# Optimization experiments

Measured on AMD Instinct MI355X. Metric: run time of the kernel, lower is better.

The kernel has to match this reference:

```python
import jax, jax.numpy as jnp
import numpy as np
from jax import lax

PRE_NMS = 2000
POST_NMS = 300
NMS_THRESH = 0.7
MIN_SIZE = 16.0
SCALE = 1.0
RATIOS = (0.5, 1.0, 2.0)
SCALES = (8, 16, 32)
STRIDES = (8, 16, 32)
FEAT_HW = ((100, 100), (50, 50), (25, 25))
BASE_SIZE = 16.0


def _anchor_base(scale):
    py = px = BASE_SIZE / 2.0
    ab = np.zeros((len(RATIOS), 4), dtype=np.float32)
    for i, r in enumerate(RATIOS):
        h = BASE_SIZE * scale * np.sqrt(r)
        w = BASE_SIZE * scale * np.sqrt(1.0 / r)
        ab[i] = [py - h / 2.0, px - w / 2.0, py + h / 2.0, px + w / 2.0]
    return ab


def _enum_anchors():
    out = []
    for lvl in range(3):
        ab = _anchor_base(SCALES[lvl])
        hh, ww = FEAT_HW[lvl]
        fs = STRIDES[lvl]
        sy = np.arange(0, hh * fs, fs)
        sx = np.arange(0, ww * fs, fs)
        sx, sy = np.meshgrid(sx, sy)
        shift = np.stack((sy.ravel(), sx.ravel(), sy.ravel(), sx.ravel()), axis=1)
        a = ab[None, :, :] + shift[:, None, :]  # [K, A, 4]
        out.append(a.reshape(-1, 4).astype(np.float32))
    return np.concatenate(out, axis=0)  # [39375, 4]


def setup_inputs() -> dict:
    key = jax.random.key(0)
    ks = jax.random.split(key, 8)
    inp = {
        "feat0": jax.random.normal(ks[0], (2, 256, 100, 100), jnp.float32),
        "feat1": jax.random.normal(ks[1], (2, 256, 50, 50), jnp.float32),
        "feat2": jax.random.normal(ks[2], (2, 256, 25, 25), jnp.float32),
        "conv_w": 0.01 * jax.random.normal(ks[3], (256, 256, 3, 3), jnp.float32),
        "conv_b": jnp.zeros((256,), jnp.float32),
        "score_w": 0.01 * jax.random.normal(ks[4], (6, 256), jnp.float32),
        "score_b": jnp.zeros((6,), jnp.float32),
        "loc_w": 0.01 * jax.random.normal(ks[5], (12, 256), jnp.float32),
        "loc_b": jnp.zeros((12,), jnp.float32),
        "anchors": jnp.asarray(_enum_anchors()),
        "img_h": 800,
        "img_w": 800,
    }
    return inp


def loc2bbox(anchors, loc):
    src_h = anchors[:, 2] - anchors[:, 0]
    src_w = anchors[:, 3] - anchors[:, 1]
    ctr_y = anchors[:, 0] + 0.5 * src_h
    ctr_x = anchors[:, 1] + 0.5 * src_w
    dy, dx, dh, dw = loc[:, 0], loc[:, 1], loc[:, 2], loc[:, 3]
    cy = dy * src_h + ctr_y
    cx = dx * src_w + ctr_x
    h = jnp.exp(dh) * src_h
    w = jnp.exp(dw) * src_w
    return jnp.stack([cy - 0.5 * h, cx - 0.5 * w, cy + 0.5 * h, cx + 0.5 * w], axis=1)


def _iou_matrix(boxes):
    area = (boxes[:, 2] - boxes[:, 0]) * (boxes[:, 3] - boxes[:, 1])
    tl = jnp.maximum(boxes[:, None, :2], boxes[None, :, :2])
    br = jnp.minimum(boxes[:, None, 2:], boxes[None, :, 2:])
    wh = jnp.clip(br - tl, 0.0)
    inter = wh[..., 0] * wh[..., 1]
    return inter / (area[:, None] + area[None, :] - inter + 1e-12)


def _nms_keep(boxes, valid):
    # greedy NMS over score-sorted boxes; returns boolean keep mask
    M = _iou_matrix(boxes)  # [PRE_NMS, PRE_NMS]
    idx = jnp.arange(PRE_NMS)

    def body(i, suppressed):
        sup_later = (~suppressed[i]) & (M[i] > NMS_THRESH) & (idx > i)
        return suppressed | sup_later

    suppressed = lax.fori_loop(0, PRE_NMS, body, ~valid)
    return ~suppressed


def _propose(loc, fg, anchors, img_h, img_w):
    roi = loc2bbox(anchors, loc)  # [S, 4]
    roi = jnp.stack([
        jnp.clip(roi[:, 0], 0.0, float(img_h)),
        jnp.clip(roi[:, 1], 0.0, float(img_w)),
        jnp.clip(roi[:, 2], 0.0, float(img_h)),
        jnp.clip(roi[:, 3], 0.0, float(img_w)),
    ], axis=1)
    hs = roi[:, 2] - roi[:, 0]
    ws = roi[:, 3] - roi[:, 1]
    valid = (hs >= MIN_SIZE * SCALE) & (ws >= MIN_SIZE * SCALE)
    sc = jnp.where(valid, fg, -jnp.inf)
    top_sc, top_idx = lax.top_k(sc, PRE_NMS)
    boxes = roi[top_idx]
    keep = _nms_keep(boxes, jnp.isfinite(top_sc))
    # stable move of kept boxes to the front (indices are unique)
    order = jnp.argsort(jnp.where(keep, jnp.arange(PRE_NMS), PRE_NMS))[:POST_NMS]
    rois = boxes[order] * keep[order][:, None].astype(boxes.dtype)  # zero-pad invalid
    return rois  # [POST_NMS, 4]


def reference(feat0, feat1, feat2, conv_w, conv_b, score_w, score_b, loc_w, loc_b, anchors, img_h, img_w):
    feats = [feat0, feat1, feat2]
    n = feat0.shape[0]
    locs, scores, fgs = [], [], []
    dn = ("NCHW", "OIHW", "NCHW")
    for x in feats:
        h = jax.nn.relu(
            lax.conv_general_dilated(x, conv_w, (1, 1), "SAME", dimension_numbers=dn)
            + conv_b[None, :, None, None]
        )
        hh, ww = h.shape[2], h.shape[3]
        loc = jnp.einsum("nchw,oc->nhwo", h, loc_w) + loc_b  # [n,h,w,12]
        sc = jnp.einsum("nchw,oc->nhwo", h, score_w) + score_b  # [n,h,w,6]
        fg = jax.nn.softmax(sc.reshape(n, hh, ww, 3, 2), axis=-1)[..., 1]
        locs.append(loc.reshape(n, -1, 4))
        scores.append(sc.reshape(n, -1, 2))
        fgs.append(fg.reshape(n, -1))
    rpn_locs = jnp.concatenate(locs, axis=1)      # [n, S, 4]
    rpn_scores = jnp.concatenate(scores, axis=1)  # [n, S, 2]
    rpn_fg = jnp.concatenate(fgs, axis=1)         # [n, S]
    rois = jax.vmap(lambda l, f: _propose(l, f, anchors, img_h, img_w))(rpn_locs, rpn_fg)
    rois = rois.reshape(-1, 4)  # [n*POST_NMS, 4]
    roi_indices = jnp.repeat(jnp.arange(n, dtype=jnp.int32), POST_NMS)
    return rpn_locs, rpn_scores, rois, roi_indices, anchors
```

## Files before the change

### kernel.cpp

```cpp
#include <hip/hip_runtime.h>
#include <hip/hip_fp16.h>
#include <cstdint>
#include <cstddef>

typedef unsigned long long u64;
typedef unsigned int u32;
typedef __attribute__((ext_vector_type(8))) _Float16 f16x8;
typedef __attribute__((ext_vector_type(4))) float f32x4;

#define NANCHORS 39375
#define PRE_NMS  2000
#define POST_NMS 300
#define CAND_CAP 4096
#define MPAD 2048
#define UNEG 0x007FFFFFu
#define NPIX 26250

__device__ __forceinline__ u32 f2u(float f) {
  u32 u = __float_as_uint(f);
  return (u & 0x80000000u) ? ~u : (u | 0x80000000u);
}

#define GLOAD16(gp, lp) __builtin_amdgcn_global_load_lds( \
    (const __attribute__((address_space(1))) u32*)(const void*)(gp), \
    (__attribute__((address_space(3))) u32*)(void*)(lp), 16, 0, 0)

#define DPP_SUM16(v) do { \
  v += __int_as_float(__builtin_amdgcn_update_dpp(0, __float_as_int(v), 0x128, 0xf, 0xf, true)); \
  v += __int_as_float(__builtin_amdgcn_update_dpp(0, __float_as_int(v), 0x124, 0xf, 0xf, true)); \
  v += __int_as_float(__builtin_amdgcn_update_dpp(0, __float_as_int(v), 0x122, 0xf, 0xf, true)); \
  v += __int_as_float(__builtin_amdgcn_update_dpp(0, __float_as_int(v), 0x121, 0xf, 0xf, true)); \
} while (0)

__global__ __launch_bounds__(256) void prep_kernel(
    const float* __restrict__ f0, const float* __restrict__ f1, const float* __restrict__ f2,
    const float* __restrict__ w, const float* __restrict__ anchors,
    short* __restrict__ xh, short* __restrict__ xl,
    short* __restrict__ wh, short* __restrict__ wl,
    float* __restrict__ out_anchors)
{
  int blk = blockIdx.x;
  int tid = threadIdx.x;
  if (blk < 1656) {
    __shared__ float tile[64][65];
    int t = blk;
    int HW, W, W2, np; const float* fp; int AB, ABS;
    if (t < 1256)      { HW = 10000; W = 100; W2 = 102; np = 157; fp = f0; AB = 0;       ABS = 2663424; }
    else if (t < 1576) { t -= 1256; HW = 2500; W = 50; W2 = 52; np = 40; fp = f1; AB = 5326848; ABS = 692224; }
    else               { t -= 1576; HW = 625;  W = 25; W2 = 27; np = 10; fp = f2; AB = 6711296; ABS = 186624; }
    int posb = t % np, r = t / np;
    int ci0 = (r & 3) * 64, b = r >> 2;
    int pos0 = posb * 64;
    int lane = tid & 63, wv = tid >> 6;
    int rp = pos0 + lane; if (rp >= HW) rp = HW - 1;
    const float* src = fp + (size_t)(b * 256 + ci0) * HW;
#pragma unroll
    for (int p = 0; p < 16; ++p) {
      int cl = wv * 16 + p;
      tile[cl][lane] = src[(size_t)cl * HW + rp];
    }
    __syncthreads();
    int pix = tid >> 2, cq = tid & 3;
    int pos = pos0 + pix;
    if (pos < HW) {
      int y = pos / W, x = pos - y * W;
      size_t ob = (size_t)AB + (size_t)b * ABS + ((size_t)((y + 1) * W2 + (x + 1))) * 256 + ci0 + cq * 16;
      __align__(16) short hs[16], ls[16];
#pragma unroll
      for (int j = 0; j < 16; ++j) {
        float v = tile[cq * 16 + j][pix];
        __half h = __float2half(v);
        __half l = __float2half((v - __half2float(h)) * 2048.0f);
        hs[j] = __half_as_short(h);
        ls[j] = __half_as_short(l);
      }
      *(int4*)(xh + ob) = ((int4*)hs)[0];
      *(int4*)(xh + ob + 8) = ((int4*)hs)[1];
      *(int4*)(xl + ob) = ((int4*)ls)[0];
      *(int4*)(xl + ob + 8) = ((int4*)ls)[1];
    }
  } else if (blk < 3960) {
    int idx = (blk - 1656) * 256 + tid;
    int tap = idx >> 16, co = (idx >> 8) & 255, ci = idx & 255;
    float v = w[(size_t)co * 2304 + ci * 9 + tap];
    __half h = __float2half(v);
    __half l = __float2half((v - __half2float(h)) * 2048.0f);
    wh[idx] = __half_as_short(h);
    wl[idx] = __half_as_short(l);
  } else if (blk < 4316) {
    int g = (blk - 3960) * 256 + tid;
    int t = g >> 6, ln = g & 63;
    int b = t / 712, i = t % 712;
    int W2, AB, ABS;
    if (i < 404)      { W2 = 102; AB = 0;       ABS = 2663424; }
    else if (i < 608) { i -= 404; W2 = 52; AB = 5326848; ABS = 692224; }
    else              { i -= 608; W2 = 27; AB = 6711296; ABS = 186624; }
    int y, x;
    if (i < W2)          { y = 0;      x = i; }
    else if (i < 2 * W2) { y = W2 - 1; x = i - W2; }
    else { int j = i - 2 * W2; y = 1 + (j >> 1); x = (j & 1) ? (W2 - 1) : 0; }
    size_t base = (size_t)AB + (size_t)b * ABS + ((size_t)(y * W2 + x)) * 256 + ln * 4;
    int2 z = {0, 0};
    *(int2*)(xh + base) = z;
    *(int2*)(xl + base) = z;
  } else {
    int t = (blk - 4316) * 256 + tid;
    if (t < 157500) out_anchors[t] = anchors[t];
  }
}

__global__ __launch_bounds__(256, 2) void gemmconv_kernel(
    const short* __restrict__ xh, const short* __restrict__ xl,
    const short* __restrict__ wh, const short* __restrict__ wl,
    const float* __restrict__ bias,
    const float* __restrict__ loc_w, const float* __restrict__ score_w,
    float* __restrict__ proj2)
{
  __shared__ __align__(16) short smem[32768];

  int lb = (blockIdx.x & 7) * 52 + (blockIdx.x >> 3);
  int HW, W, W2, AB, ABS, lvlbase;
  if (lb < 316)      { HW = 10000; W = 100; W2 = 102; AB = 0;       ABS = 2663424; lvlbase = 0; }
  else if (lb < 396) { lb -= 316; HW = 2500; W = 50; W2 = 52; AB = 5326848; ABS = 692224; lvlbase = 10000; }
  else               { lb -= 396; HW = 625;  W = 25; W2 = 27; AB = 6711296; ABS = 186624; lvlbase = 12500; }
  int mb = lb >> 2, b = (lb >> 1) & 1, nb = lb & 1;
  int pos0 = mb * 128, co0 = nb * 128;

  int tid = threadIdx.x;
  int s = tid & 7, mrow = tid >> 3;
  int aoff[4], boff[4];
#pragma unroll
  for (int i = 0; i < 4; ++i) {
    int m = i * 32 + mrow;
    int pos = pos0 + m; if (pos >= HW) pos = HW - 1;
    int y = pos / W, x = pos - y * W;
    aoff[i] = AB + b * ABS + (y * W2 + x) * 256 + ((s ^ (m & 7)) << 3);
    boff[i] = ((co0 + m) << 8) + ((s ^ (m & 7)) << 3);
  }
  int wv = tid >> 6, lane = tid & 63;
  int lr = lane & 15, lk = lane >> 4;
  int wr = wv >> 1, wc = wv & 1;
  int rA0 = wr * 64 + lr, rB0 = wc * 64 + lr;
  int cs = (lr & 7) << 4;
  int c0 = ((lk * 16) ^ cs) >> 1;
  int c1 = ((64 + lk * 16) ^ cs) >> 1;

  f32x4 acc1[4][4], acc2[4][4];
  f32x4 zro = {0.f, 0.f, 0.f, 0.f};
#pragma unroll
  for (int i = 0; i < 4; ++i)
#pragma unroll
    for (int j = 0; j < 4; ++j) { acc1[i][j] = zro; acc2[i][j] = zro; }

  for (int cc = 0; cc < 36; ++cc) {
    int tap = cc >> 2, cq = cc & 3;
    int ty = tap / 3, tx = tap - ty * 3;
    int adel = (ty * W2 + tx) * 256 + (cq << 6);
    int bdel = (tap << 16) + (cq << 6);
    if (cc) __syncthreads();
#pragma unroll
    for (int i = 0; i < 4; ++i) {
      int d = i * 2048 + wv * 512;
      GLOAD16(xh + aoff[i] + adel, smem + d);
      GLOAD16(xl + aoff[i] + adel, smem + 8192 + d);
      GLOAD16(wh + boff[i] + bdel, smem + 16384 + d);
      GLOAD16(wl + boff[i] + bdel, smem + 24576 + d);
    }
    __syncthreads();
#pragma unroll
    for (int k2 = 0; k2 < 2; ++k2) {
      int ck = k2 ? c1 : c0;
      f16x8 ah[4], al[4], bh[4], bl[4];
#pragma unroll
      for (int q = 0; q < 4; ++q) {
        int ro = (rA0 + q * 16) * 64 + ck;
        ah[q] = *(const f16x8*)(smem + ro);
        al[q] = *(const f16x8*)(smem + 8192 + ro);
        int rb = (rB0 + q * 16) * 64 + ck;
        bh[q] = *(const f16x8*)(smem + 16384 + rb);
        bl[q] = *(const f16x8*)(smem + 24576 + rb);
      }
#pragma unroll
      for (int m4 = 0; m4 < 4; ++m4)
#pragma unroll
        for (int n4 = 0; n4 < 4; ++n4) {
          acc1[m4][n4] = __builtin_amdgcn_mfma_f32_16x16x32_f16(ah[m4], bh[n4], acc1[m4][n4], 0, 0, 0);
          acc2[m4][n4] = __builtin_amdgcn_mfma_f32_16x16x32_f16(ah[m4], bl[n4], acc2[m4][n4], 0, 0, 0);
          acc2[m4][n4] = __builtin_amdgcn_mfma_f32_16x16x32_f16(al[m4], bh[n4], acc2[m4][n4], 0, 0, 0);
        }
    }
  }

  float br[4];
#pragma unroll
  for (int n4 = 0; n4 < 4; ++n4) br[n4] = bias[co0 + wc * 64 + n4 * 16 + lr];
  float* pslot = proj2 + (size_t)(nb * 2 + wc) * NPIX * 20;
  int Pbase = b * 13125 + lvlbase;

#pragma unroll 1
  for (int half = 0; half < 2; ++half) {
    float wpr[4][9];
#pragma unroll
    for (int n4 = 0; n4 < 4; ++n4) {
      int c = co0 + wc * 64 + n4 * 16 + lr;
#pragma unroll
      for (int oo = 0; oo < 9; ++oo) {
        int o = half * 9 + oo;
        wpr[n4][oo] = (o < 12) ? loc_w[o * 256 + c] : score_w[(o - 12) * 256 + c];
      }
    }
#pragma unroll
    for (int m4 = 0; m4 < 4; ++m4) {
#pragma unroll
      for (int j = 0; j < 4; ++j) {
        int pos = pos0 + wr * 64 + m4 * 16 + lk * 4 + j;
        bool ok = pos < HW;
        float po[9];
#pragma unroll
        for (int oo = 0; oo < 9; ++oo) po[oo] = 0.f;
#pragma unroll
        for (int n4 = 0; n4 < 4; ++n4) {
          float h = acc1[m4][n4][j] + acc2[m4][n4][j] * 4.8828125e-4f + br[n4];
          h = ok ? fmaxf(h, 0.f) : 0.f;
#pragma unroll
          for (int oo = 0; oo < 9; ++oo) po[oo] = fmaf(h, wpr[n4][oo], po[oo]);
        }
#pragma unroll
        for (int oo = 0; oo < 9; ++oo) DPP_SUM16(po[oo]);
        if (ok && lr < 9) {
          float out = po[0];
#pragma unroll
          for (int oo = 1; oo < 9; ++oo) if (lr == oo) out = po[oo];
          pslot[(size_t)(Pbase + pos) * 20 + half * 9 + lr] = out;
        }
      }
    }
  }
}

__global__ __launch_bounds__(256) void decode_kernel(
    const float* __restrict__ proj2, const float* __restrict__ loc_b, const float* __restrict__ score_b,
    const float* __restrict__ anchors, const int* __restrict__ imgh, const int* __restrict__ imgw,
    float* __restrict__ out_locs, float* __restrict__ out_scores,
    float* __restrict__ boxes, u32* __restrict__ ukey)
{
  int P = blockIdx.x * 256 + threadIdx.x;
  if (P >= NPIX) return;
  int b = P / 13125, r = P % 13125;
  int pos, base_row;
  if (r < 10000)      { pos = r;         base_row = 0; }
  else if (r < 12500) { pos = r - 10000; base_row = 30000; }
  else                { pos = r - 12500; base_row = 37500; }

  float sarr[18];
#pragma unroll
  for (int o = 0; o < 18; ++o)
    sarr[o] = proj2[(size_t)P * 20 + o] + proj2[(size_t)NPIX * 20 + (size_t)P * 20 + o]
            + proj2[(size_t)2 * NPIX * 20 + (size_t)P * 20 + o]
            + proj2[(size_t)3 * NPIX * 20 + (size_t)P * 20 + o];

  float IH = (float)(*imgh), IW = (float)(*imgw);
#pragma unroll
  for (int a = 0; a < 3; ++a) {
    float l0 = sarr[4 * a + 0] + loc_b[4 * a + 0];
    float l1 = sarr[4 * a + 1] + loc_b[4 * a + 1];
    float l2 = sarr[4 * a + 2] + loc_b[4 * a + 2];
    float l3 = sarr[4 * a + 3] + loc_b[4 * a + 3];
    float sc0 = sarr[12 + 2 * a + 0] + score_b[2 * a + 0];
    float sc1 = sarr[12 + 2 * a + 1] + score_b[2 * a + 1];

    int row = base_row + pos * 3 + a;
    size_t g = (size_t)b * NANCHORS + row;
    *(float4*)(out_locs + g * 4) = make_float4(l0, l1, l2, l3);
    out_scores[g * 2 + 0] = sc0; out_scores[g * 2 + 1] = sc1;

    float mx = fmaxf(sc0, sc1);
    float e0 = expf(sc0 - mx), e1 = expf(sc1 - mx);
    float fg = e1 / (e0 + e1);

    const float* an = anchors + (size_t)row * 4;
    float a0 = an[0], a1 = an[1], a2 = an[2], a3 = an[3];
    float sh = a2 - a0, sw = a3 - a1;
    float cy = a0 + 0.5f * sh, cx = a1 + 0.5f * sw;
    float ncy = l0 * sh + cy, ncx = l1 * sw + cx;
    float nh = expf(l2) * sh, nw = expf(l3) * sw;
    float y1 = fminf(fmaxf(ncy - 0.5f * nh, 0.f), IH);
    float x1 = fminf(fmaxf(ncx - 0.5f * nw, 0.f), IW);
    float y2 = fminf(fmaxf(ncy + 0.5f * nh, 0.f), IH);
    float x2 = fminf(fmaxf(ncx + 0.5f * nw, 0.f), IW);
    bool valid = ((y2 - y1) >= 16.0f) && ((x2 - x1) >= 16.0f);
    float scm = valid ? fg : -__builtin_inff();

    *(float4*)(boxes + g * 4) = make_float4(y1, x1, y2, x2);
    ukey[g] = f2u(scm);
  }
}

__global__ __launch_bounds__(1024) void selectsort_kernel(
    const u32* __restrict__ ukey, const float* __restrict__ boxes,
    float* __restrict__ topbox, u64* __restrict__ sup0)
{
  int b = blockIdx.x, tid = threadIdx.x;
  int lane = tid & 63;
  const u32* u = ukey + (size_t)b * NANCHORS;
  __shared__ u32 hist[256];
  __shared__ u32 sh_prefix;
  __shared__ int sh_rem;
  __shared__ int sh_cnt;
  __shared__ u64 key[CAND_CAP];
  __shared__ unsigned char validf[2048];

  u32 val[39];
#pragma unroll
  for (int k = 0; k < 38; ++k) val[k] = u[tid + k * 1024];
  val[38] = (tid < 463) ? u[tid + 38912] : 0u;

  u32 prefix = 0; int rem = PRE_NMS;
#pragma unroll 1
  for (int pass = 0; pass < 4; ++pass) {
    int shift = 24 - 8 * pass;
    if (tid < 256) hist[tid] = 0;
    __syncthreads();
    u32 himask = (pass == 0) ? 0u : (0xFFFFFFFFu << (shift + 8));
    u32 pmask = prefix & himask;
#pragma unroll
    for (int k = 0; k < 39; ++k) {
      bool live = (k < 38) || (tid < 463);
      u32 v = val[k];
      bool m = live && ((v & himask) == pmask);
      u32 bin = (v >> shift) & 255u;
      u64 actm = __ballot(m);
      if (actm) {
        int src = __ffsll(actm) - 1;
        u32 binf = __shfl(bin, src, 64);
        bool same = m && (bin == binf);
        u64 sm = __ballot(same);
        if (same) {
          if (lane == __ffsll(sm) - 1)
            atomicAdd(&hist[binf], (u32)__popcll(sm));
        } else if (m) {
          atomicAdd(&hist[bin], 1u);
        }
      }
    }
    __syncthreads();
    if (tid < 64) {
      u32 h0 = hist[4 * lane], h1 = hist[4 * lane + 1];
      u32 h2 = hist[4 * lane + 2], h3 = hist[4 * lane + 3];
      u32 L = h0 + h1 + h2 + h3;
      u32 SS = L;
#pragma unroll
      for (int off = 1; off < 64; off <<= 1) {
        u32 tv = __shfl_down(SS, off, 64);
        if (lane + off < 64) SS += tv;
      }
      u32 T = SS - L;
      u32 s3 = h3 + T, s2 = h2 + s3, s1 = h1 + s2, s0 = h0 + s1;
      u32 sv[5] = {s0, s1, s2, s3, T};
#pragma unroll
      for (int j = 0; j < 4; ++j) {
        if ((int)sv[j] >= rem && (int)sv[j + 1] < rem) {
          sh_prefix = prefix | ((u32)(4 * lane + j) << shift);
          sh_rem = rem - (int)sv[j + 1];
        }
      }
    }
    __syncthreads();
    prefix = sh_prefix; rem = sh_rem;
  }

  if (tid == 0) sh_cnt = 0;
  __syncthreads();
#pragma unroll
  for (int k = 0; k < 39; ++k) {
    bool live = (k < 38) || (tid < 463);
    u32 v = val[k];
    bool c = live && (v >= prefix);
    u64 mask = __ballot(c);
    if (mask) {
      int leader = __ffsll(mask) - 1;
      int cntw = __popcll(mask);
      int base = 0;
      if (lane == leader) base = atomicAdd(&sh_cnt, cntw);
      base = __shfl(base, leader, 64);
      int p = base + (int)__popcll(mask & ((1ull << lane) - 1ull));
      if (c && p < CAND_CAP)
        key[p] = ((u64)v << 32) | (u32)(~(u32)(tid + k * 1024));
    }
  }
  __syncthreads();
  int cnt = (sh_cnt < CAND_CAP) ? sh_cnt : CAND_CAP;
  for (int t = tid; t < CAND_CAP; t += 1024)
    if (t >= cnt) key[t] = 0ull;
  __syncthreads();

  u32 n = (cnt <= 2048) ? 2048u : (u32)CAND_CAP;
  for (u32 k = 2; k <= n; k <<= 1) {
    for (u32 j = k >> 1; j > 0; j >>= 1) {
      __syncthreads();
      for (u32 t = tid; t < n; t += 1024) {
        u32 ixj = t ^ j;
        if (ixj > t) {
          u64 a = key[t], c = key[ixj];
          bool desc = ((t & k) == 0);
          if (desc ? (a < c) : (a > c)) { key[t] = c; key[ixj] = a; }
        }
      }
    }
  }
  __syncthreads();

  for (int t = tid; t < 2048; t += 1024) {
    unsigned char vf = 0;
    if (t < PRE_NMS) {
      u64 kk = key[t];
      u32 uu = (u32)(kk >> 32);
      float* tb = topbox + ((size_t)b * PRE_NMS + t) * 4;
      if (uu != 0u) {
        u32 idx = ~((u32)kk);
        const float* bp = boxes + ((size_t)b * NANCHORS + idx) * 4;
        tb[0] = bp[0]; tb[1] = bp[1]; tb[2] = bp[2]; tb[3] = bp[3];
        vf = (uu != UNEG) ? 1 : 0;
      } else {
        tb[0] = 0.f; tb[1] = 0.f; tb[2] = 0.f; tb[3] = 0.f;
      }
    }
    validf[t] = vf;
  }
  __syncthreads();
  if (tid < 32) {
    u64 m = 0;
    for (int bit = 0; bit < 64; ++bit) {
      int j = tid * 64 + bit;
      if (j >= PRE_NMS || !validf[j]) m |= (1ull << bit);
    }
    sup0[b * 32 + tid] = m;
  }
}

__global__ __launch_bounds__(256) void iou_kernel(const float* __restrict__ topbox, u32* __restrict__ M32)
{
  __shared__ float4 bx[64];
  int b = blockIdx.y;
  int w = blockIdx.x >> 3;
  int i = (blockIdx.x & 7) * 256 + threadIdx.x;
  const float4* tb = (const float4*)(topbox + (size_t)b * PRE_NMS * 4);
  if (threadIdx.x < 64) {
    int j = w * 64 + threadIdx.x;
    bx[threadIdx.x] = (j < PRE_NMS) ? tb[j] : make_float4(0.f, 0.f, 0.f, 0.f);
  }
  __syncthreads();
  if (i >= PRE_NMS) return;
  float4 bi = tb[i];
  float iy1 = bi.x, ix1 = bi.y, iy2 = bi.z, ix2 = bi.w;
  float ai = (iy2 - iy1) * (ix2 - ix1);
  u64 m = 0;
#pragma unroll 8
  for (int bit = 0; bit < 64; ++bit) {
    int j = w * 64 + bit;
    if (j < PRE_NMS && j > i) {
      float4 bj = bx[bit];
      float ty = fmaxf(iy1, bj.x), tx = fmaxf(ix1, bj.y);
      float by = fminf(iy2, bj.z), bxx = fminf(ix2, bj.w);
      float hh = fmaxf(by - ty, 0.f), ww = fmaxf(bxx - tx, 0.f);
      float inter = hh * ww;
      float aj = (bj.z - bj.x) * (bj.w - bj.y);
      float iou = inter / (ai + aj - inter + 1e-12f);
      if (iou > 0.7f) m |= (1ull << bit);
    }
  }
  u32* out = M32 + (size_t)b * MPAD * 64;
  out[(size_t)(2 * w)     * MPAD + i] = (u32)m;
  out[(size_t)(2 * w + 1) * MPAD + i] = (u32)(m >> 32);
}

__global__ __launch_bounds__(320) void final_kernel(
    const u32* __restrict__ M32, const u64* __restrict__ sup0, const float* __restrict__ topbox,
    float* __restrict__ rois, float* __restrict__ roiidx)
{
  int b = blockIdx.x, tid = threadIdx.x;
  __shared__ u32 supl[64];
  __shared__ int ord[POST_NMS];
  __shared__ int cnt_s;

  if (tid < 64) {
    int l = tid;
    const u32* col = M32 + (size_t)b * MPAD * 64 + (size_t)l * MPAD;
    u32 sup = ((const u32*)sup0)[b * 64 + l];
    uint4 A[16], B[16];
#pragma unroll
    for (int k = 0; k < 16; ++k) A[k] = *(const uint4*)(col + 4 * k);

#define NMS_PROC(buf, cc) do {                                                     \
  _Pragma("unroll")                                                                \
  for (int rr = 0; rr < 64; ++rr) {                                                \
    u32 d = ((rr & 3) == 0) ? buf[rr >> 2].x : ((rr & 3) == 1) ? buf[rr >> 2].y :  \
            ((rr & 3) == 2) ? buf[rr >> 2].z : buf[rr >> 2].w;                     \
    u32 sb = (u32)__builtin_amdgcn_readlane((int)sup, 2 * (cc) + (rr >> 5));       \
    u32 m = ((sb >> (rr & 31)) & 1u) - 1u;                                         \
    sup |= m & d;                                                                  \
  } } while (0)

    for (int c = 0; c < 32; c += 2) {
#pragma unroll
      for (int k = 0; k < 16; ++k) B[k] = *(const uint4*)(col + (c + 1) * 64 + 4 * k);
      NMS_PROC(A, c);
      if (c + 2 < 32) {
#pragma unroll
        for (int k = 0; k < 16; ++k) A[k] = *(const uint4*)(col + (c + 2) * 64 + 4 * k);
      }
      NMS_PROC(B, c + 1);
    }
    supl[l] = sup;
  }
  __syncthreads();
  if (tid == 0) {
    int cnt = 0;
    for (int w = 0; w < 64 && cnt < POST_NMS; ++w) {
      u32 kept = ~supl[w];
      while (kept && cnt < POST_NMS) {
        int bit = __builtin_ctz(kept); kept &= kept - 1;
        ord[cnt++] = w * 32 + bit;
      }
    }
    cnt_s = cnt;
  }
  __syncthreads();
  if (tid < POST_NMS) {
    float v0 = 0.f, v1 = 0.f, v2 = 0.f, v3 = 0.f;
    if (tid < cnt_s) {
      const float* tb = topbox + ((size_t)b * PRE_NMS + ord[tid]) * 4;
      v0 = tb[0]; v1 = tb[1]; v2 = tb[2]; v3 = tb[3];
    }
    float* r = rois + ((size_t)b * POST_NMS + tid) * 4;
    r[0] = v0; r[1] = v1; r[2] = v2; r[3] = v3;
    roiidx[b * POST_NMS + tid] = (float)b;
  }
}

extern "C" void kernel_launch(void* const* d_in, const int* in_sizes, int n_in,
                              void* d_out, int out_size, void* d_ws, size_t ws_size,
                              hipStream_t stream) {
  const float* feat0   = (const float*)d_in[0];
  const float* feat1   = (const float*)d_in[1];
  const float* feat2   = (const float*)d_in[2];
  const float* conv_w  = (const float*)d_in[3];
  const float* conv_b  = (const float*)d_in[4];
  const float* score_w = (const float*)d_in[5];
  const float* score_b = (const float*)d_in[6];
  const float* loc_w   = (const float*)d_in[7];
  const float* loc_b   = (const float*)d_in[8];
  const float* anchors = (const float*)d_in[9];
  const int*   img_h   = (const int*)d_in[10];
  const int*   img_w   = (const int*)d_in[11];

  float* out_f       = (float*)d_out;
  float* out_locs    = out_f;
  float* out_scores  = out_f + 315000;
  float* out_rois    = out_f + 472500;
  float* out_roiidx  = out_f + 474900;
  float* out_anchors = out_f + 475500;

  char* p = (char*)d_ws;
  short* xth = (short*)p;     p += (size_t)7084544 * 2;
  short* xtl = (short*)p;     p += (size_t)7084544 * 2;
  short* wsh = (short*)p;     p += (size_t)589824 * 2;
  short* wsl = (short*)p;     p += (size_t)589824 * 2;
  float* proj2 = (float*)p;   p += (size_t)4 * NPIX * 20 * 4;
  float* boxes = (float*)p;   p += (size_t)315000 * 4;
  u32* ukey = (u32*)p;        p += (size_t)78752 * 4;
  float* topbox = (float*)p;  p += (size_t)16000 * 4;
  u32* M32 = (u32*)p;         p += (size_t)2 * MPAD * 64 * 4;
  u64* sup0 = (u64*)p;        p += 64 * 8;

  prep_kernel<<<4932, 256, 0, stream>>>(
      feat0, feat1, feat2, conv_w, anchors, xth, xtl, wsh, wsl, out_anchors);
  gemmconv_kernel<<<416, 256, 0, stream>>>(xth, xtl, wsh, wsl, conv_b, loc_w, score_w, proj2);
  decode_kernel<<<(NPIX + 255) / 256, 256, 0, stream>>>(
      proj2, loc_b, score_b, anchors, img_h, img_w,
      out_locs, out_scores, boxes, ukey);
  selectsort_kernel<<<2, 1024, 0, stream>>>(ukey, boxes, topbox, sup0);
  iou_kernel<<<dim3(256, 2), 256, 0, stream>>>(topbox, M32);
  final_kernel<<<2, 320, 0, stream>>>(M32, sup0, topbox, out_rois, out_roiidx);
}
```

Measured before the change: 348.6 us.

## Split top-k select-sort into multi-block histogram, scan, compact, and rank kernels

```diff
diff --git a/kernel.cpp b/kernel.cpp
--- a/kernel.cpp
+++ b/kernel.cpp
@@ -37,7 +37,9 @@
     const float* __restrict__ w, const float* __restrict__ anchors,
     short* __restrict__ xh, short* __restrict__ xl,
     short* __restrict__ wh, short* __restrict__ wl,
-    float* __restrict__ out_anchors)
+    float* __restrict__ out_anchors,
+    u32* __restrict__ ghist16, u32* __restrict__ ghist24, u32* __restrict__ gticket,
+    u64* __restrict__ sup0, float* __restrict__ topbox)
 {
   int blk = blockIdx.x;
   int tid = threadIdx.x;
@@ -103,9 +105,19 @@
     int2 z = {0, 0};
     *(int2*)(xh + base) = z;
     *(int2*)(xl + base) = z;
-  } else {
+  } else if (blk < 4932) {
     int t = (blk - 4316) * 256 + tid;
     if (t < 157500) out_anchors[t] = anchors[t];
+  } else if (blk < 5060) {
+    int t = (blk - 4932) * 256 + tid;
+    ((int4*)ghist16)[t] = make_int4(0, 0, 0, 0);
+  } else if (blk < 5076) {
+    int t = (blk - 5060) * 256 + tid;
+    ((int4*)topbox)[t] = make_int4(0, 0, 0, 0);
+  } else {
+    if (tid < 64) sup0[tid] = ~0ull;
+    else if (tid < 192) ((int4*)ghist24)[tid - 64] = make_int4(0, 0, 0, 0);
+    else if (tid == 192) { gticket[0] = 0; gticket[1] = 0; }
   }
 }
 
@@ -296,145 +308,129 @@
   }
 }
 
-__global__ __launch_bounds__(1024) void selectsort_kernel(
-    const u32* __restrict__ ukey, const float* __restrict__ boxes,
-    float* __restrict__ topbox, u64* __restrict__ sup0)
-{
-  int b = blockIdx.x, tid = threadIdx.x;
-  int lane = tid & 63;
+__global__ __launch_bounds__(256) void selhist_kernel(
+    const u32* __restrict__ ukey, u32* __restrict__ ghist16)
+{
+  int b = blockIdx.y, lane = threadIdx.x & 63;
   const u32* u = ukey + (size_t)b * NANCHORS;
-  __shared__ u32 hist[256];
-  __shared__ u32 sh_prefix;
-  __shared__ int sh_rem;
-  __shared__ int sh_cnt;
-  __shared__ u64 key[CAND_CAP];
-  __shared__ unsigned char validf[2048];
-
-  u32 val[39];
-#pragma unroll
-  for (int k = 0; k < 38; ++k) val[k] = u[tid + k * 1024];
-  val[38] = (tid < 463) ? u[tid + 38912] : 0u;
-
-  u32 prefix = 0; int rem = PRE_NMS;
-#pragma unroll 1
-  for (int pass = 0; pass < 4; ++pass) {
-    int shift = 24 - 8 * pass;
-    if (tid < 256) hist[tid] = 0;
-    __syncthreads();
-    u32 himask = (pass == 0) ? 0u : (0xFFFFFFFFu << (shift + 8));
-    u32 pmask = prefix & himask;
-#pragma unroll
-    for (int k = 0; k < 39; ++k) {
-      bool live = (k < 38) || (tid < 463);
-      u32 v = val[k];
-      bool m = live && ((v & himask) == pmask);
-      u32 bin = (v >> shift) & 255u;
-      u64 actm = __ballot(m);
-      if (actm) {
-        int src = __ffsll(actm) - 1;
-        u32 binf = __shfl(bin, src, 64);
-        bool same = m && (bin == binf);
-        u64 sm = __ballot(same);
-        if (same) {
-          if (lane == __ffsll(sm) - 1)
-            atomicAdd(&hist[binf], (u32)__popcll(sm));
-        } else if (m) {
-          atomicAdd(&hist[bin], 1u);
-        }
-      }
-    }
-    __syncthreads();
-    if (tid < 64) {
-      u32 h0 = hist[4 * lane], h1 = hist[4 * lane + 1];
-      u32 h2 = hist[4 * lane + 2], h3 = hist[4 * lane + 3];
-      u32 L = h0 + h1 + h2 + h3;
-      u32 SS = L;
-#pragma unroll
-      for (int off = 1; off < 64; off <<= 1) {
-        u32 tv = __shfl_down(SS, off, 64);
-        if (lane + off < 64) SS += tv;
-      }
-      u32 T = SS - L;
-      u32 s3 = h3 + T, s2 = h2 + s3, s1 = h1 + s2, s0 = h0 + s1;
-      u32 sv[5] = {s0, s1, s2, s3, T};
-#pragma unroll
-      for (int j = 0; j < 4; ++j) {
-        if ((int)sv[j] >= rem && (int)sv[j + 1] < rem) {
-          sh_prefix = prefix | ((u32)(4 * lane + j) << shift);
-          sh_rem = rem - (int)sv[j + 1];
-        }
-      }
-    }
-    __syncthreads();
-    prefix = sh_prefix; rem = sh_rem;
-  }
-
-  if (tid == 0) sh_cnt = 0;
+  u32* h = ghist16 + (size_t)b * 65536;
+  for (int i = blockIdx.x * 256 + threadIdx.x; i < NANCHORS; i += 64 * 256) {
+    u32 bin = u[i] >> 16;
+    u64 act = __ballot(true);
+    int src = __ffsll(act) - 1;
+    u32 binf = __shfl(bin, src, 64);
+    bool same = (bin == binf);
+    u64 sm = __ballot(same);
+    if (same) {
+      if (lane == src) atomicAdd(&h[binf], (u32)__popcll(sm));
+    } else {
+      atomicAdd(&h[bin], 1u);
+    }
+  }
+}
+
+__global__ __launch_bounds__(1024) void selscan_kernel(
+    const u32* __restrict__ ghist16, u32* __restrict__ gcut)
+{
+  int b = blockIdx.x, tid = threadIdx.x, lane = tid & 63, wv = tid >> 6;
+  const u32* h = ghist16 + (size_t)b * 65536;
+  __shared__ u32 wsum[16];
+  u32 tot = 0;
+#pragma unroll 8
+  for (int j = 0; j < 64; ++j) tot += h[tid * 64 + j];
+  u32 SS = tot;
+#pragma unroll
+  for (int off = 1; off < 64; off <<= 1) {
+    u32 tv = __shfl_down(SS, off, 64);
+    if (lane + off < 64) SS += tv;
+  }
+  if (lane == 0) wsum[wv] = SS;
   __syncthreads();
-#pragma unroll
-  for (int k = 0; k < 39; ++k) {
-    bool live = (k < 38) || (tid < 463);
-    u32 v = val[k];
-    bool c = live && (v >= prefix);
+  u32 above_waves = 0;
+  for (int w2 = wv + 1; w2 < 16; ++w2) above_waves += wsum[w2];
+  u32 cumAbove = above_waves + (SS - tot);
+  u32 s = cumAbove;
+  for (int j = 63; j >= 0; --j) {
+    u32 nxt = s;
+    s += h[tid * 64 + j];
+    if (s >= (u32)PRE_NMS && nxt < (u32)PRE_NMS) {
+      gcut[b * 2] = (u32)(tid * 64 + j);
+      gcut[b * 2 + 1] = nxt;
+    }
+  }
+}
+
+__global__ __launch_bounds__(256) void selcompact_kernel(
+    const u32* __restrict__ ukey, const u32* __restrict__ gcut,
+    u64* __restrict__ cand, u32* __restrict__ gticket, u32* __restrict__ ghist24)
+{
+  int b = blockIdx.y, lane = threadIdx.x & 63;
+  const u32* u = ukey + (size_t)b * NANCHORS;
+  u32 T16 = gcut[b * 2];
+  for (int i = blockIdx.x * 256 + threadIdx.x; i < NANCHORS; i += 64 * 256) {
+    u32 v = u[i];
+    u32 hi = v >> 16;
+    if (hi == T16) atomicAdd(&ghist24[b * 256 + ((v >> 8) & 255u)], 1u);
+    bool c = (hi >= T16);
     u64 mask = __ballot(c);
     if (mask) {
       int leader = __ffsll(mask) - 1;
-      int cntw = __popcll(mask);
-      int base = 0;
-      if (lane == leader) base = atomicAdd(&sh_cnt, cntw);
+      u32 base = 0;
+      if (lane == leader) base = atomicAdd(&gticket[b], (u32)__popcll(mask));
       base = __shfl(base, leader, 64);
-      int p = base + (int)__popcll(mask & ((1ull << lane) - 1ull));
+      int p = (int)base + (int)__popcll(mask & ((1ull << lane) - 1ull));
       if (c && p < CAND_CAP)
-        key[p] = ((u64)v << 32) | (u32)(~(u32)(tid + k * 1024));
-    }
-  }
+        cand[(size_t)b * CAND_CAP + p] = ((u64)v << 32) | (u32)(~(u32)i);
+    }
+  }
+}
+
+__global__ __launch_bounds__(256) void rank_kernel(
+    const u64* __restrict__ cand, const u32* __restrict__ gticket,
+    const u32* __restrict__ gcut, const u32* __restrict__ ghist24,
+    const float* __restrict__ boxes, float* __restrict__ topbox, u64* __restrict__ sup0)
+{
+  __shared__ u64 cds[CAND_CAP];
+  __shared__ u32 sh_cut24;
+  int b = blockIdx.y, tid = threadIdx.x, lane = tid & 63;
+  u32 T16 = gcut[b * 2], C1 = gcut[b * 2 + 1];
+  if (tid < 64) {
+    u32 h0 = ghist24[b * 256 + 4 * lane],     h1 = ghist24[b * 256 + 4 * lane + 1];
+    u32 h2 = ghist24[b * 256 + 4 * lane + 2], h3 = ghist24[b * 256 + 4 * lane + 3];
+    u32 L = h0 + h1 + h2 + h3;
+    u32 SS = L;
+#pragma unroll
+    for (int off = 1; off < 64; off <<= 1) {
+      u32 tv = __shfl_down(SS, off, 64);
+      if (lane + off < 64) SS += tv;
+    }
+    u32 T = SS - L;
+    u32 s3 = h3 + T, s2 = h2 + s3, s1 = h1 + s2, s0 = h0 + s1;
+    u32 sv[5] = {s0, s1, s2, s3, T};
+#pragma unroll
+    for (int j = 0; j < 4; ++j) {
+      if (C1 + sv[j] >= (u32)PRE_NMS && C1 + sv[j + 1] < (u32)PRE_NMS)
+        sh_cut24 = (T16 << 8) | (u32)(4 * lane + j);
+    }
+  }
+  int C = (int)gticket[b]; if (C > CAND_CAP) C = CAND_CAP;
+  const u64* cd = cand + (size_t)b * CAND_CAP;
+  for (int t = tid; t < C; t += 256) cds[t] = cd[t];
   __syncthreads();
-  int cnt = (sh_cnt < CAND_CAP) ? sh_cnt : CAND_CAP;
-  for (int t = tid; t < CAND_CAP; t += 1024)
-    if (t >= cnt) key[t] = 0ull;
-  __syncthreads();
-
-  u32 n = (cnt <= 2048) ? 2048u : (u32)CAND_CAP;
-  for (u32 k = 2; k <= n; k <<= 1) {
-    for (u32 j = k >> 1; j > 0; j >>= 1) {
-      __syncthreads();
-      for (u32 t = tid; t < n; t += 1024) {
-        u32 ixj = t ^ j;
-        if (ixj > t) {
-          u64 a = key[t], c = key[ixj];
-          bool desc = ((t & k) == 0);
-          if (desc ? (a < c) : (a > c)) { key[t] = c; key[ixj] = a; }
-        }
-      }
-    }
-  }
-  __syncthreads();
-
-  for (int t = tid; t < 2048; t += 1024) {
-    unsigned char vf = 0;
-    if (t < PRE_NMS) {
-      u64 kk = key[t];
-      u32 uu = (u32)(kk >> 32);
-      float* tb = topbox + ((size_t)b * PRE_NMS + t) * 4;
-      if (uu != 0u) {
-        u32 idx = ~((u32)kk);
-        const float* bp = boxes + ((size_t)b * NANCHORS + idx) * 4;
-        tb[0] = bp[0]; tb[1] = bp[1]; tb[2] = bp[2]; tb[3] = bp[3];
-        vf = (uu != UNEG) ? 1 : 0;
-      } else {
-        tb[0] = 0.f; tb[1] = 0.f; tb[2] = 0.f; tb[3] = 0.f;
-      }
-    }
-    validf[t] = vf;
-  }
-  __syncthreads();
-  if (tid < 32) {
-    u64 m = 0;
-    for (int bit = 0; bit < 64; ++bit) {
-      int j = tid * 64 + bit;
-      if (j >= PRE_NMS || !validf[j]) m |= (1ull << bit);
-    }
-    sup0[b * 32 + tid] = m;
+  u32 cut24 = sh_cut24;
+
+  int i = blockIdx.x * 256 + tid;
+  if (i >= C) return;
+  u64 me = cds[i];
+  u32 k = (u32)(me >> 32);
+  if ((k >> 8) < cut24 || k == UNEG) return;
+  int rank = 0;
+  for (int j = 0; j < C; ++j) rank += (cds[j] > me) ? 1 : 0;
+  if (rank < PRE_NMS) {
+    u32 idx = ~((u32)me);
+    float4 bb = *(const float4*)(boxes + ((size_t)b * NANCHORS + idx) * 4);
+    *(float4*)(topbox + ((size_t)b * PRE_NMS + rank) * 4) = bb;
+    atomicAnd((u64*)&sup0[b * 32 + (rank >> 6)], ~(1ull << (rank & 63)));
   }
 }
 
@@ -572,14 +568,23 @@
   float* topbox = (float*)p;  p += (size_t)16000 * 4;
   u32* M32 = (u32*)p;         p += (size_t)2 * MPAD * 64 * 4;
   u64* sup0 = (u64*)p;        p += 64 * 8;
-
-  prep_kernel<<<4932, 256, 0, stream>>>(
-      feat0, feat1, feat2, conv_w, anchors, xth, xtl, wsh, wsl, out_anchors);
+  u64* cand = (u64*)p;        p += (size_t)2 * CAND_CAP * 8;
+  u32* ghist16 = (u32*)p;     p += (size_t)2 * 65536 * 4;
+  u32* ghist24 = (u32*)p;     p += (size_t)2 * 256 * 4;
+  u32* gcut = (u32*)p;        p += 16;
+  u32* gticket = (u32*)p;     p += 16;
+
+  prep_kernel<<<5077, 256, 0, stream>>>(
+      feat0, feat1, feat2, conv_w, anchors, xth, xtl, wsh, wsl, out_anchors,
+      ghist16, ghist24, gticket, sup0, topbox);
   gemmconv_kernel<<<416, 256, 0, stream>>>(xth, xtl, wsh, wsl, conv_b, loc_w, score_w, proj2);
   decode_kernel<<<(NPIX + 255) / 256, 256, 0, stream>>>(
       proj2, loc_b, score_b, anchors, img_h, img_w,
       out_locs, out_scores, boxes, ukey);
-  selectsort_kernel<<<2, 1024, 0, stream>>>(ukey, boxes, topbox, sup0);
+  selhist_kernel<<<dim3(64, 2), 256, 0, stream>>>(ukey, ghist16);
+  selscan_kernel<<<2, 1024, 0, stream>>>(ghist16, gcut);
+  selcompact_kernel<<<dim3(64, 2), 256, 0, stream>>>(ukey, gcut, cand, gticket, ghist24);
+  rank_kernel<<<dim3(16, 2), 256, 0, stream>>>(cand, gticket, gcut, ghist24, boxes, topbox, sup0);
   iou_kernel<<<dim3(256, 2), 256, 0, stream>>>(topbox, M32);
   final_kernel<<<2, 320, 0, stream>>>(M32, sup0, topbox, out_rois, out_roiidx);
 }
```

Result: slower. 452.1 us (+29.7%).
